# Performance work log

Measured on AMD Instinct MI355X. Metric: run time of the kernel, lower is better.

Reference implementation:

```python
import jax, jax.numpy as jnp
import numpy as np

V = 256        # vocab (bytes)
DM = 1024      # d_model
NL = 8         # num layers
N = 16         # d_state
K = 4          # d_conv
E = 2 * DM     # d_inner (expand=2)
R = DM // 16   # dt_rank = 64
EPS = 1e-5
B, T = 1, 1024


def setup_inputs() -> dict:
    key = jax.random.key(0)
    ks = jax.random.split(key, 10)
    s = lambda i, shape, scale=0.02: jax.random.normal(ks[i], shape, jnp.float32) * scale
    A_init = jnp.log(jnp.tile(jnp.arange(1, N + 1, dtype=jnp.float32), (NL, E, 1)))
    return {
        "input_ids": jax.random.randint(ks[0], (B, T), 0, V),
        "embed": s(1, (V, DM)),
        "Wxz": s(2, (NL, DM, 2 * E)),            # in_proj (no bias)
        "conv_w": s(3, (NL, E, K), 0.1),          # depthwise causal conv
        "conv_b": jnp.zeros((NL, E), jnp.float32),
        "Wx": s(4, (NL, E, R + 2 * N)),           # x_proj -> dt, B, C
        "Wdt": s(5, (NL, R, E), 0.1),             # dt_proj
        "dt_bias": jnp.full((NL, E), -4.6, jnp.float32),  # softplus(-4.6) ~ 0.01
        "A_log": A_init,                          # A = -exp(A_log), S4D-real init
        "D": jnp.ones((NL, E), jnp.float32),      # skip connection
        "Wout": s(6, (NL, E, DM)),                # out_proj (no bias)
        "norm_w": jnp.ones((NL, DM), jnp.float32),
        "final_norm_w": jnp.ones((DM,), jnp.float32),
        "lm_head_w": s(7, (DM, V)),               # lm_head (no bias)
    }


def rmsnorm(x, w):
    return x * jax.lax.rsqrt(jnp.mean(x * x, axis=-1, keepdims=True) + EPS) * w


def selective_scan(x, dt, A, Bm, Cm, Dp):
    # x, dt: [B,T,E]; A: [E,N]; Bm, Cm: [B,T,N]; Dp: [E]
    dA = jnp.exp(dt[..., None] * A)                              # [B,T,E,N]
    dBx = dt[..., None] * Bm[:, :, None, :] * x[..., None]       # [B,T,E,N]

    def step(h, inp):
        dA_t, dBx_t, C_t = inp                                   # [B,E,N],[B,E,N],[B,N]
        h = dA_t * h + dBx_t
        y = jnp.einsum('ben,bn->be', h, C_t)
        return h, y

    h0 = jnp.zeros((x.shape[0], E, N), x.dtype)
    _, ys = jax.lax.scan(step, h0, (dA.transpose(1, 0, 2, 3),
                                    dBx.transpose(1, 0, 2, 3),
                                    Cm.transpose(1, 0, 2)))
    return ys.transpose(1, 0, 2) + Dp * x                        # [B,T,E]


def mamba_layer(h, p):
    Wxz, cw, cb, Wx, Wdt, dtb, A_log, Dp, Wout, nw = p
    res = h
    u = rmsnorm(h, nw)
    xz = u @ Wxz                                                 # [B,T,2E]
    x, z = jnp.split(xz, 2, axis=-1)
    # causal depthwise conv over time
    xc = jax.lax.conv_general_dilated(x.transpose(0, 2, 1), cw[:, None, :],
                                      (1,), [(K - 1, 0)], feature_group_count=E)
    x = jax.nn.silu(xc.transpose(0, 2, 1) + cb)                  # [B,T,E]
    xdbl = x @ Wx                                                # [B,T,R+2N]
    dt = jax.nn.softplus(xdbl[..., :R] @ Wdt + dtb)              # [B,T,E]
    Bm = xdbl[..., R:R + N]
    Cm = xdbl[..., R + N:]
    A = -jnp.exp(A_log)                                          # [E,N]
    y = selective_scan(x, dt, A, Bm, Cm, Dp)
    y = y * jax.nn.silu(z)
    return res + y @ Wout, None


def reference(input_ids, embed, Wxz, conv_w, conv_b, Wx, Wdt, dt_bias, A_log, D,
              Wout, norm_w, final_norm_w, lm_head_w):
    h = embed[input_ids]                                         # [B,T,DM]
    h, _ = jax.lax.scan(mamba_layer, h,
                        (Wxz, conv_w, conv_b, Wx, Wdt, dt_bias, A_log, D, Wout, norm_w))
    h = rmsnorm(h, final_norm_w)
    return h @ lm_head_w                                         # logits [B,T,V]
```

## Files before the change

### kernel.cpp

```cpp
#include <hip/hip_runtime.h>
#include <hip/hip_bf16.h>

#define DM_   1024
#define NLAY  8
#define NST   16
#define KCONV 4
#define EE    2048
#define E2    4096
#define RNK   64
#define SEQ   1024
#define NXD   96
#define VOC   256
#define EPS_  1e-5f
#define NCH   32
#define CLEN  32

typedef __attribute__((ext_vector_type(8))) short bf16x8;
typedef __attribute__((ext_vector_type(4))) float f32x4;
typedef __hip_bfloat16 bf16;

__device__ __forceinline__ float sigmoidf_(float x){ return 1.f/(1.f+__expf(-x)); }
__device__ __forceinline__ float siluf_(float x){ return x*sigmoidf_(x); }
__device__ __forceinline__ float softplusf_(float x){ return (x>15.f)?x:log1pf(__expf(x)); }

__device__ __forceinline__ void gld_lds16(const short* g, short* lds_uniform){
  __builtin_amdgcn_global_load_lds(
      (const __attribute__((address_space(1))) unsigned int*)(const void*)g,
      (__attribute__((address_space(3))) unsigned int*)(void*)lds_uniform,
      16, 0, 0);
}

__global__ void k_transpose_bf16(const float* __restrict__ in, bf16* __restrict__ out,
                                 int rows, int cols, long in_stride, long out_stride){
  __shared__ float tile[32][33];
  const float* inp = in + (size_t)blockIdx.z * in_stride;
  bf16* outp = out + (size_t)blockIdx.z * out_stride;
  int c0 = blockIdx.x*32, r0 = blockIdx.y*32;
  int tx = threadIdx.x, ty = threadIdx.y;
#pragma unroll
  for (int j = 0; j < 4; j++)
    tile[ty + j*8][tx] = inp[(size_t)(r0 + ty + j*8)*cols + c0 + tx];
  __syncthreads();
#pragma unroll
  for (int j = 0; j < 4; j++)
    outp[(size_t)(c0 + ty + j*8)*rows + r0 + tx] = __float2bfloat16(tile[tx][ty + j*8]);
}

__global__ void k_rmsnorm_fuse(const int* __restrict__ ids, const float* __restrict__ emb,
                               float* __restrict__ h, const float* __restrict__ s0,
                               const float* __restrict__ s1, const float* __restrict__ w,
                               bf16* __restrict__ u){
  int t = blockIdx.x;
  float* hp = h + (size_t)t*DM_;
  float v[4];
  float ss = 0.f;
#pragma unroll
  for (int j = 0; j < 4; j++){
    int i = threadIdx.x + j*256;
    float x;
    if (ids){ x = emb[(size_t)ids[t]*DM_ + i]; hp[i] = x; }
    else if (s0){ x = hp[i] + s0[(size_t)t*DM_ + i] + s1[(size_t)t*DM_ + i]; hp[i] = x; }
    else { x = hp[i]; }
    v[j] = x; ss += x*x;
  }
#pragma unroll
  for (int o = 32; o > 0; o >>= 1) ss += __shfl_down(ss, o, 64);
  __shared__ float red[4];
  if ((threadIdx.x & 63) == 0) red[threadIdx.x >> 6] = ss;
  __syncthreads();
  float tot = red[0]+red[1]+red[2]+red[3];
  float sc = rsqrtf(tot*(1.f/DM_) + EPS_);
  bf16* up = u + (size_t)t*DM_;
#pragma unroll
  for (int j = 0; j < 4; j++){
    int i = threadIdx.x + j*256;
    up[i] = __float2bfloat16(v[j]*sc*w[i]);
  }
}

template<int BM, int BN, int NWM, int NWN, int MODE>
__global__ __launch_bounds__(256) void k_gemm(
    const short* __restrict__ A, const short* __restrict__ Bt, float* __restrict__ C,
    int M, int N, int K, int Ksplit, const float* __restrict__ bias)
{
  constexpr int BK = 64;
  constexpr int WM = BM/NWM, WN = BN/NWN;
  constexpr int MT = WM/16, NT = WN/16;
  constexpr int ABY = BM*BK*2, BBY = BN*BK*2;
  constexpr int AISS = ABY/4096, BISS = BBY/4096;
  __shared__ __align__(16) short As[2][BM*BK];
  __shared__ __align__(16) short Bs[2][BN*BK];
  int tid = threadIdx.x, lane = tid & 63, wave = tid >> 6;
  int wr = wave / NWN, wc = wave % NWN;
  int m0 = blockIdx.x * BM, n0 = blockIdx.y * BN;
  int lrow = lane & 15, lq = lane >> 4;
  int wbase = (tid & ~63) * 16;

  int kbeg = blockIdx.z * Ksplit;
  int nk = Ksplit / BK;

  f32x4 acc[MT][NT];
#pragma unroll
  for (int i = 0; i < MT; i++)
#pragma unroll
    for (int j = 0; j < NT; j++) acc[i][j] = (f32x4){0.f,0.f,0.f,0.f};

  auto stage = [&](int k0, int buf){
#pragma unroll
    for (int i = 0; i < AISS; i++){
      int off = i*4096 + tid*16;
      int row = off >> 7;
      int kc  = ((off >> 4) & 7) ^ (row & 7);
      gld_lds16(A + (size_t)(m0+row)*K + k0 + kc*8,
                As[buf] + ((i*4096 + wbase) >> 1));
    }
#pragma unroll
    for (int i = 0; i < BISS; i++){
      int off = i*4096 + tid*16;
      int row = off >> 7;
      int kc  = ((off >> 4) & 7) ^ (row & 7);
      gld_lds16(Bt + (size_t)(n0+row)*K + k0 + kc*8,
                Bs[buf] + ((i*4096 + wbase) >> 1));
    }
  };

  stage(kbeg, 0);
  __syncthreads();
  for (int it = 0; it < nk; it++){
    int cur = it & 1;
    if (it + 1 < nk) stage(kbeg + (it+1)*BK, cur ^ 1);
#pragma unroll
    for (int s = 0; s < 2; s++){
      bf16x8 af[MT], bfr[NT];
#pragma unroll
      for (int mt = 0; mt < MT; mt++){
        int row = wr*WM + mt*16 + lrow;
        int cc = (s*4 + lq) ^ (row & 7);
        af[mt] = *(const bf16x8*)(As[cur] + row*BK + cc*8);
      }
#pragma unroll
      for (int nt = 0; nt < NT; nt++){
        int row = wc*WN + nt*16 + lrow;
        int cc = (s*4 + lq) ^ (row & 7);
        bfr[nt] = *(const bf16x8*)(Bs[cur] + row*BK + cc*8);
      }
#pragma unroll
      for (int mt = 0; mt < MT; mt++)
#pragma unroll
        for (int nt = 0; nt < NT; nt++)
          acc[mt][nt] = __builtin_amdgcn_mfma_f32_16x16x32_bf16(af[mt], bfr[nt], acc[mt][nt], 0,0,0);
    }
    __syncthreads();
  }

  size_t slab = (MODE == 4) ? (size_t)blockIdx.z * M * N : 0;
#pragma unroll
  for (int mt = 0; mt < MT; mt++){
    int row = m0 + wr*WM + mt*16 + lq*4;
#pragma unroll
    for (int nt = 0; nt < NT; nt++){
      int col = n0 + wc*WN + nt*16 + lrow;
#pragma unroll
      for (int r = 0; r < 4; r++){
        float v = acc[mt][nt][r];
        size_t idx = slab + (size_t)(row + r)*N + col;
        if (MODE == 1) C[idx] = softplusf_(v + bias[col]);
        else C[idx] = v;
      }
    }
  }
}

__global__ void k_conv_silu(const float* __restrict__ xz, const float* __restrict__ cw,
                            const float* __restrict__ cb, float* __restrict__ xact,
                            bf16* __restrict__ xbf){
  int t = blockIdx.y;
  int e = blockIdx.x*256 + threadIdx.x;
  float4 w4 = *(const float4*)(cw + (size_t)e*4);
  float acc = cb[e];
  if (t >= 3){
    acc += xz[(size_t)(t-3)*E2 + e]*w4.x + xz[(size_t)(t-2)*E2 + e]*w4.y
         + xz[(size_t)(t-1)*E2 + e]*w4.z + xz[(size_t)t*E2 + e]*w4.w;
  } else {
    const float* wp = (const float*)&w4;
#pragma unroll
    for (int k = 0; k < 4; k++){ int tt = t-3+k; if (tt >= 0) acc += xz[(size_t)tt*E2 + e]*wp[k]; }
  }
  float xv = siluf_(acc);
  xact[(size_t)t*EE + e] = xv;
  xbf[(size_t)t*EE + e] = __float2bfloat16(xv);
}

__global__ void k_reduce_xdbl(const float* __restrict__ s, float* __restrict__ out,
                              bf16* __restrict__ out64){
  int i = blockIdx.x*256 + threadIdx.x;
  float v = 0.f;
#pragma unroll
  for (int c = 0; c < 8; c++) v += s[(size_t)c*SEQ*NXD + i];
  out[i] = v;
  int t = i / NXD, cc = i - t*NXD;
  if (cc < RNK) out64[(size_t)t*RNK + cc] = __float2bfloat16(v);
}

__global__ void k_reduce_lm(const float* __restrict__ s, float* __restrict__ out){
  int i = blockIdx.x*256 + threadIdx.x;
  float v = 0.f;
#pragma unroll
  for (int c = 0; c < 4; c++) v += s[(size_t)c*SEQ*VOC + i];
  out[i] = v;
}

__global__ void k_scanA(const float* __restrict__ dt, const float* __restrict__ x,
                        const float* __restrict__ xdbl, const float* __restrict__ Alog,
                        float* __restrict__ S, float* __restrict__ dtsum){
  int e = blockIdx.x*256 + threadIdx.x;
  int c = blockIdx.y;
  int t0 = c*CLEN;
  float Ae[NST];
#pragma unroll
  for (int n = 0; n < NST; n++) Ae[n] = -__expf(Alog[(size_t)e*NST + n]);
  __shared__ float Bsm[CLEN][NST];
  for (int i = threadIdx.x; i < CLEN*NST; i += 256)
    Bsm[i>>4][i&15] = xdbl[(size_t)(t0 + (i>>4))*NXD + RNK + (i&15)];
  __syncthreads();
  float h[NST];
#pragma unroll
  for (int n = 0; n < NST; n++) h[n] = 0.f;
  float ds = 0.f;
  for (int tt = 0; tt < CLEN; tt++){
    float dtv = dt[(size_t)(t0+tt)*EE + e];
    float xv  = x[(size_t)(t0+tt)*EE + e];
    ds += dtv;
    float sx = dtv * xv;
#pragma unroll
    for (int n = 0; n < NST; n++)
      h[n] = __expf(dtv*Ae[n])*h[n] + sx*Bsm[tt][n];
  }
  float* Sp = S + ((size_t)c*EE + e)*NST;
#pragma unroll
  for (int n = 0; n < NST; n++) Sp[n] = h[n];
  dtsum[(size_t)c*EE + e] = ds;
}

__global__ void k_scanB(const float* __restrict__ S, const float* __restrict__ dtsum,
                        const float* __restrict__ Alog, float* __restrict__ hinit){
  int idx = blockIdx.x*256 + threadIdx.x;
  float An = -__expf(Alog[idx]);
  int e = idx >> 4;
  float h = 0.f;
  for (int c = 0; c < NCH; c++){
    hinit[(size_t)c*EE*NST + idx] = h;
    h = __expf(dtsum[(size_t)c*EE + e]*An)*h + S[(size_t)c*EE*NST + idx];
  }
}

__global__ void k_scanC(const float* __restrict__ dt, const float* __restrict__ x,
                        const float* __restrict__ xdbl, const float* __restrict__ Alog,
                        const float* __restrict__ Dp, const float* __restrict__ hinit,
                        const float* __restrict__ xz, bf16* __restrict__ ybf){
  int e = blockIdx.x*256 + threadIdx.x;
  int c = blockIdx.y;
  int t0 = c*CLEN;
  float Ae[NST];
#pragma unroll
  for (int n = 0; n < NST; n++) Ae[n] = -__expf(Alog[(size_t)e*NST + n]);
  __shared__ float Bsm[CLEN][NST], Csm[CLEN][NST];
  for (int i = threadIdx.x; i < CLEN*NST; i += 256){
    int tt = i>>4, n = i&15;
    Bsm[tt][n] = xdbl[(size_t)(t0+tt)*NXD + RNK + n];
    Csm[tt][n] = xdbl[(size_t)(t0+tt)*NXD + RNK + NST + n];
  }
  __syncthreads();
  float h[NST];
  const float* hp = hinit + ((size_t)c*EE + e)*NST;
#pragma unroll
  for (int n = 0; n < NST; n++) h[n] = hp[n];
  float Dv = Dp[e];
  for (int tt = 0; tt < CLEN; tt++){
    float dtv = dt[(size_t)(t0+tt)*EE + e];
    float xv  = x[(size_t)(t0+tt)*EE + e];
    float sx = dtv*xv;
    float y = Dv*xv;
#pragma unroll
    for (int n = 0; n < NST; n++){
      h[n] = __expf(dtv*Ae[n])*h[n] + sx*Bsm[tt][n];
      y += h[n]*Csm[tt][n];
    }
    float zv = xz[(size_t)(t0+tt)*E2 + EE + e];
    y *= zv*sigmoidf_(zv);
    ybf[(size_t)(t0+tt)*EE + e] = __float2bfloat16(y);
  }
}

extern "C" void kernel_launch(void* const* d_in, const int* in_sizes, int n_in,
                              void* d_out, int out_size, void* d_ws, size_t ws_size,
                              hipStream_t stream)
{
  const int*   ids  = (const int*)d_in[0];
  const float* emb  = (const float*)d_in[1];
  const float* Wxz  = (const float*)d_in[2];
  const float* cw   = (const float*)d_in[3];
  const float* cb   = (const float*)d_in[4];
  const float* Wx   = (const float*)d_in[5];
  const float* Wdt  = (const float*)d_in[6];
  const float* dtb  = (const float*)d_in[7];
  const float* Alog = (const float*)d_in[8];
  const float* Dp   = (const float*)d_in[9];
  const float* Wout = (const float*)d_in[10];
  const float* nw   = (const float*)d_in[11];
  const float* fnw  = (const float*)d_in[12];
  const float* lmw  = (const float*)d_in[13];

  char* p = (char*)d_ws;
  auto alloc = [&](size_t bytes){ void* r = (void*)p; p += (bytes + 255) & ~(size_t)255; return r; };
  bf16* wxz_bf  = (bf16*)alloc((size_t)NLAY*E2*DM_*2);
  bf16* wout_bf = (bf16*)alloc((size_t)NLAY*DM_*EE*2);
  bf16* wx_bf   = (bf16*)alloc((size_t)NLAY*NXD*EE*2);
  bf16* wdt_bf  = (bf16*)alloc((size_t)NLAY*EE*RNK*2);
  bf16* lm_bf   = (bf16*)alloc((size_t)VOC*DM_*2);
  float* h      = (float*)alloc((size_t)SEQ*DM_*4);
  float* hslab  = (float*)alloc((size_t)2*SEQ*DM_*4);
  bf16* u_bf    = (bf16*)alloc((size_t)SEQ*DM_*2);
  float* xzb    = (float*)alloc((size_t)SEQ*E2*4);
  float* xact   = (float*)alloc((size_t)SEQ*EE*4);
  bf16* x_bf    = (bf16*)alloc((size_t)SEQ*EE*2);
  float* xdbl_s = (float*)alloc((size_t)8*SEQ*NXD*4);
  float* xdbl   = (float*)alloc((size_t)SEQ*NXD*4);
  bf16* xd64    = (bf16*)alloc((size_t)SEQ*RNK*2);
  float* dtbuf  = (float*)alloc((size_t)SEQ*EE*4);
  float* Sbuf   = (float*)alloc((size_t)NCH*EE*NST*4);
  float* dtsum  = (float*)alloc((size_t)NCH*EE*4);
  float* hinit  = (float*)alloc((size_t)NCH*EE*NST*4);
  bf16* y_bf    = (bf16*)alloc((size_t)SEQ*EE*2);
  float* lmslab = (float*)alloc((size_t)4*SEQ*VOC*4);

  k_transpose_bf16<<<dim3(E2/32, DM_/32, NLAY), dim3(32,8), 0, stream>>>(Wxz, wxz_bf, DM_, E2, (long)DM_*E2, (long)E2*DM_);
  k_transpose_bf16<<<dim3(DM_/32, EE/32, NLAY), dim3(32,8), 0, stream>>>(Wout, wout_bf, EE, DM_, (long)EE*DM_, (long)DM_*EE);
  k_transpose_bf16<<<dim3(NXD/32, EE/32, NLAY), dim3(32,8), 0, stream>>>(Wx, wx_bf, EE, NXD, (long)EE*NXD, (long)NXD*EE);
  k_transpose_bf16<<<dim3(EE/32, RNK/32, NLAY), dim3(32,8), 0, stream>>>(Wdt, wdt_bf, RNK, EE, (long)RNK*EE, (long)EE*RNK);
  k_transpose_bf16<<<dim3(VOC/32, DM_/32, 1), dim3(32,8), 0, stream>>>(lmw, lm_bf, DM_, VOC, 0, 0);

  for (int l = 0; l < NLAY; l++){
    k_rmsnorm_fuse<<<SEQ, 256, 0, stream>>>(
        l == 0 ? ids : nullptr, emb, h,
        l == 0 ? nullptr : hslab, hslab + (size_t)SEQ*DM_,
        nw + (size_t)l*DM_, u_bf);
    k_gemm<128,64,2,2,0><<<dim3(SEQ/128, E2/64, 1), 256, 0, stream>>>(
        (const short*)u_bf, (const short*)(wxz_bf + (size_t)l*E2*DM_), xzb,
        SEQ, E2, DM_, DM_, nullptr);
    k_conv_silu<<<dim3(EE/256, SEQ), 256, 0, stream>>>(
        xzb, cw + (size_t)l*EE*KCONV, cb + (size_t)l*EE, xact, x_bf);
    k_gemm<32,96,2,2,4><<<dim3(SEQ/32, 1, 8), 256, 0, stream>>>(
        (const short*)x_bf, (const short*)(wx_bf + (size_t)l*NXD*EE), xdbl_s,
        SEQ, NXD, EE, EE/8, nullptr);
    k_reduce_xdbl<<<SEQ*NXD/256, 256, 0, stream>>>(xdbl_s, xdbl, xd64);
    k_gemm<64,64,2,2,1><<<dim3(SEQ/64, EE/64, 1), 256, 0, stream>>>(
        (const short*)xd64, (const short*)(wdt_bf + (size_t)l*EE*RNK), dtbuf,
        SEQ, EE, RNK, RNK, dtb + (size_t)l*EE);
    k_scanA<<<dim3(EE/256, NCH), 256, 0, stream>>>(
        dtbuf, xact, xdbl, Alog + (size_t)l*EE*NST, Sbuf, dtsum);
    k_scanB<<<dim3(EE*NST/256), 256, 0, stream>>>(Sbuf, dtsum, Alog + (size_t)l*EE*NST, hinit);
    k_scanC<<<dim3(EE/256, NCH), 256, 0, stream>>>(
        dtbuf, xact, xdbl, Alog + (size_t)l*EE*NST, Dp + (size_t)l*EE, hinit, xzb, y_bf);
    k_gemm<64,64,2,2,4><<<dim3(SEQ/64, DM_/64, 2), 256, 0, stream>>>(
        (const short*)y_bf, (const short*)(wout_bf + (size_t)l*DM_*EE), hslab,
        SEQ, DM_, EE, EE/2, nullptr);
  }
  k_rmsnorm_fuse<<<SEQ, 256, 0, stream>>>(
      nullptr, emb, h, hslab, hslab + (size_t)SEQ*DM_, fnw, u_bf);
  k_gemm<64,64,2,2,4><<<dim3(SEQ/64, VOC/64, 4), 256, 0, stream>>>(
      (const short*)u_bf, (const short*)lm_bf, lmslab,
      SEQ, VOC, DM_, DM_/4, nullptr);
  k_reduce_lm<<<SEQ*VOC/256, 256, 0, stream>>>(lmslab, (float*)d_out);
}
```

Baseline: 1.164 ms.

## Replace per-stage kernel launches with a single cooperative persistent megakernel

```diff
diff --git a/kernel.cpp b/kernel.cpp
--- a/kernel.cpp
+++ b/kernel.cpp
@@ -1,10 +1,12 @@
 #include <hip/hip_runtime.h>
 #include <hip/hip_bf16.h>
+#include <hip/hip_cooperative_groups.h>
+
+namespace cg = cooperative_groups;
 
 #define DM_   1024
 #define NLAY  8
 #define NST   16
-#define KCONV 4
 #define EE    2048
 #define E2    4096
 #define RNK   64
@@ -12,16 +14,19 @@
 #define NXD   96
 #define VOC   256
 #define EPS_  1e-5f
-#define NCH   32
-#define CLEN  32
+#define NCH   64
+#define CLEN  16
+#define NTHR  256
 
 typedef __attribute__((ext_vector_type(8))) short bf16x8;
 typedef __attribute__((ext_vector_type(4))) float f32x4;
 typedef __hip_bfloat16 bf16;
 
 __device__ __forceinline__ float sigmoidf_(float x){ return 1.f/(1.f+__expf(-x)); }
-__device__ __forceinline__ float siluf_(float x){ return x*sigmoidf_(x); }
 __device__ __forceinline__ float softplusf_(float x){ return (x>15.f)?x:log1pf(__expf(x)); }
+__device__ __forceinline__ short f2bf_s(float x){
+  union { bf16 b; short s; } cv; cv.b = __float2bfloat16(x); return cv.s;
+}
 
 __device__ __forceinline__ void gld_lds16(const short* g, short* lds_uniform){
   __builtin_amdgcn_global_load_lds(
@@ -30,97 +35,110 @@
       16, 0, 0);
 }
 
-__global__ void k_transpose_bf16(const float* __restrict__ in, bf16* __restrict__ out,
-                                 int rows, int cols, long in_stride, long out_stride){
-  __shared__ float tile[32][33];
-  const float* inp = in + (size_t)blockIdx.z * in_stride;
-  bf16* outp = out + (size_t)blockIdx.z * out_stride;
-  int c0 = blockIdx.x*32, r0 = blockIdx.y*32;
-  int tx = threadIdx.x, ty = threadIdx.y;
-#pragma unroll
-  for (int j = 0; j < 4; j++)
-    tile[ty + j*8][tx] = inp[(size_t)(r0 + ty + j*8)*cols + c0 + tx];
-  __syncthreads();
-#pragma unroll
-  for (int j = 0; j < 4; j++)
-    outp[(size_t)(c0 + ty + j*8)*rows + r0 + tx] = __float2bfloat16(tile[tx][ty + j*8]);
-}
-
-__global__ void k_rmsnorm_fuse(const int* __restrict__ ids, const float* __restrict__ emb,
-                               float* __restrict__ h, const float* __restrict__ s0,
-                               const float* __restrict__ s1, const float* __restrict__ w,
-                               bf16* __restrict__ u){
-  int t = blockIdx.x;
-  float* hp = h + (size_t)t*DM_;
-  float v[4];
-  float ss = 0.f;
-#pragma unroll
-  for (int j = 0; j < 4; j++){
-    int i = threadIdx.x + j*256;
-    float x;
-    if (ids){ x = emb[(size_t)ids[t]*DM_ + i]; hp[i] = x; }
-    else if (s0){ x = hp[i] + s0[(size_t)t*DM_ + i] + s1[(size_t)t*DM_ + i]; hp[i] = x; }
-    else { x = hp[i]; }
-    v[j] = x; ss += x*x;
-  }
-#pragma unroll
-  for (int o = 32; o > 0; o >>= 1) ss += __shfl_down(ss, o, 64);
-  __shared__ float red[4];
-  if ((threadIdx.x & 63) == 0) red[threadIdx.x >> 6] = ss;
-  __syncthreads();
-  float tot = red[0]+red[1]+red[2]+red[3];
-  float sc = rsqrtf(tot*(1.f/DM_) + EPS_);
-  bf16* up = u + (size_t)t*DM_;
-#pragma unroll
-  for (int j = 0; j < 4; j++){
-    int i = threadIdx.x + j*256;
-    up[i] = __float2bfloat16(v[j]*sc*w[i]);
-  }
-}
-
-template<int BM, int BN, int NWM, int NWN, int MODE>
-__global__ __launch_bounds__(256) void k_gemm(
-    const short* __restrict__ A, const short* __restrict__ Bt, float* __restrict__ C,
-    int M, int N, int K, int Ksplit, const float* __restrict__ bias)
+struct Params {
+  const int* ids; const float* emb; const float* Wxz; const float* cw; const float* cb;
+  const float* Wx; const float* Wdt; const float* dtb; const float* Alog; const float* Dp;
+  const float* Wout; const float* nw; const float* fnw; const float* lmw;
+  bf16 *wxz_bf, *wout_bf, *wx_bf, *wdt_bf, *lm_bf;
+  float *h, *hslab; bf16 *u_bf;
+  float *xzb, *xact; bf16 *x_bf;
+  float *xdbl, *dtbuf, *S, *dtsum;
+  bf16 *y_bf; float *out;
+};
+
+__device__ void t_job(const float* in, bf16* out, int R, int C, int L, char* smem, int gdim){
+  float (*tile)[33] = (float(*)[33])smem;
+  int tC = C >> 5, tR = R >> 5;
+  int per = tC * tR, total = per * L;
+  int tx = threadIdx.x & 31, ty = threadIdx.x >> 5;
+  for (int it = blockIdx.x; it < total; it += gdim){
+    int l = it / per, rem = it - l*per;
+    int tc = rem % tC, tr = rem / tC;
+    const float* inp = in + (size_t)l*R*C;
+    bf16* outp = out + (size_t)l*R*C;
+    int c0 = tc*32, r0 = tr*32;
+    __syncthreads();
+#pragma unroll
+    for (int j = 0; j < 4; j++)
+      tile[ty + j*8][tx] = inp[(size_t)(r0+ty+j*8)*C + c0+tx];
+    __syncthreads();
+#pragma unroll
+    for (int j = 0; j < 4; j++)
+      outp[(size_t)(c0+ty+j*8)*R + r0+tx] = __float2bfloat16(tile[tx][ty+j*8]);
+  }
+}
+
+__device__ void rms_phase(const Params& P, int mode, char* smem, int gdim){
+  float* red = (float*)smem;
+  const float* w = (mode == NLAY) ? P.fnw : (P.nw + (size_t)mode*DM_);
+  int tid = threadIdx.x;
+  for (int t = blockIdx.x; t < SEQ; t += gdim){
+    float* hp = P.h + (size_t)t*DM_;
+    float v[4]; float ss = 0.f;
+    __syncthreads();
+#pragma unroll
+    for (int j = 0; j < 4; j++){
+      int i = tid + j*256;
+      float x;
+      if (mode == 0){ x = P.emb[(size_t)P.ids[t]*DM_ + i]; hp[i] = x; }
+      else { x = hp[i] + P.hslab[(size_t)t*DM_ + i] + P.hslab[(size_t)(SEQ+t)*DM_ + i]; hp[i] = x; }
+      v[j] = x; ss += x*x;
+    }
+#pragma unroll
+    for (int o = 32; o > 0; o >>= 1) ss += __shfl_down(ss, o, 64);
+    if ((tid & 63) == 0) red[tid >> 6] = ss;
+    __syncthreads();
+    float sc = rsqrtf((red[0]+red[1]+red[2]+red[3])*(1.f/DM_) + EPS_);
+    bf16* up = P.u_bf + (size_t)t*DM_;
+#pragma unroll
+    for (int j = 0; j < 4; j++){
+      int i = tid + j*256;
+      up[i] = __float2bfloat16(v[j]*sc*w[i]);
+    }
+  }
+  if (mode == NLAY){
+    int stride = gdim*NTHR;
+    for (int i = blockIdx.x*NTHR + tid; i < SEQ*VOC; i += stride) P.out[i] = 0.f;
+  }
+}
+
+template<int BM,int BN,int NWM,int NWN>
+__device__ __forceinline__ void gemm_core(
+    const short* __restrict__ A, const short* __restrict__ Bt, int K,
+    int m0, int n0, int kbeg, int nk, short* As, short* Bs,
+    f32x4 (&acc)[(BM/NWM)/16][(BN/NWN)/16])
 {
   constexpr int BK = 64;
   constexpr int WM = BM/NWM, WN = BN/NWN;
   constexpr int MT = WM/16, NT = WN/16;
   constexpr int ABY = BM*BK*2, BBY = BN*BK*2;
   constexpr int AISS = ABY/4096, BISS = BBY/4096;
-  __shared__ __align__(16) short As[2][BM*BK];
-  __shared__ __align__(16) short Bs[2][BN*BK];
-  int tid = threadIdx.x, lane = tid & 63, wave = tid >> 6;
-  int wr = wave / NWN, wc = wave % NWN;
-  int m0 = blockIdx.x * BM, n0 = blockIdx.y * BN;
-  int lrow = lane & 15, lq = lane >> 4;
-  int wbase = (tid & ~63) * 16;
-
-  int kbeg = blockIdx.z * Ksplit;
-  int nk = Ksplit / BK;
-
-  f32x4 acc[MT][NT];
+  const int tid = threadIdx.x, lane = tid & 63, wave = tid >> 6;
+  const int wr = wave / NWN, wc = wave % NWN;
+  const int lrow = lane & 15, lq = lane >> 4;
+  const int wbase = (tid & ~63) * 16;
+
 #pragma unroll
   for (int i = 0; i < MT; i++)
 #pragma unroll
     for (int j = 0; j < NT; j++) acc[i][j] = (f32x4){0.f,0.f,0.f,0.f};
 
   auto stage = [&](int k0, int buf){
+    short* Ad = As + buf*(BM*BK);
+    short* Bd = Bs + buf*(BN*BK);
 #pragma unroll
     for (int i = 0; i < AISS; i++){
       int off = i*4096 + tid*16;
       int row = off >> 7;
       int kc  = ((off >> 4) & 7) ^ (row & 7);
-      gld_lds16(A + (size_t)(m0+row)*K + k0 + kc*8,
-                As[buf] + ((i*4096 + wbase) >> 1));
+      gld_lds16(A + (size_t)(m0+row)*K + k0 + kc*8, Ad + ((i*4096 + wbase) >> 1));
     }
 #pragma unroll
     for (int i = 0; i < BISS; i++){
       int off = i*4096 + tid*16;
       int row = off >> 7;
       int kc  = ((off >> 4) & 7) ^ (row & 7);
-      gld_lds16(Bt + (size_t)(n0+row)*K + k0 + kc*8,
-                Bs[buf] + ((i*4096 + wbase) >> 1));
+      gld_lds16(Bt + (size_t)(n0+row)*K + k0 + kc*8, Bd + ((i*4096 + wbase) >> 1));
     }
   };
 
@@ -129,6 +147,8 @@
   for (int it = 0; it < nk; it++){
     int cur = it & 1;
     if (it + 1 < nk) stage(kbeg + (it+1)*BK, cur ^ 1);
+    const short* Ac = As + cur*(BM*BK);
+    const short* Bc = Bs + cur*(BN*BK);
 #pragma unroll
     for (int s = 0; s < 2; s++){
       bf16x8 af[MT], bfr[NT];
@@ -136,13 +156,13 @@
       for (int mt = 0; mt < MT; mt++){
         int row = wr*WM + mt*16 + lrow;
         int cc = (s*4 + lq) ^ (row & 7);
-        af[mt] = *(const bf16x8*)(As[cur] + row*BK + cc*8);
+        af[mt] = *(const bf16x8*)(Ac + row*BK + cc*8);
       }
 #pragma unroll
       for (int nt = 0; nt < NT; nt++){
         int row = wc*WN + nt*16 + lrow;
         int cc = (s*4 + lq) ^ (row & 7);
-        bfr[nt] = *(const bf16x8*)(Bs[cur] + row*BK + cc*8);
+        bfr[nt] = *(const bf16x8*)(Bc + row*BK + cc*8);
       }
 #pragma unroll
       for (int mt = 0; mt < MT; mt++)
@@ -152,224 +172,360 @@
     }
     __syncthreads();
   }
-
-  size_t slab = (MODE == 4) ? (size_t)blockIdx.z * M * N : 0;
-#pragma unroll
-  for (int mt = 0; mt < MT; mt++){
-    int row = m0 + wr*WM + mt*16 + lq*4;
-#pragma unroll
-    for (int nt = 0; nt < NT; nt++){
-      int col = n0 + wc*WN + nt*16 + lrow;
-#pragma unroll
-      for (int r = 0; r < 4; r++){
-        float v = acc[mt][nt][r];
-        size_t idx = slab + (size_t)(row + r)*N + col;
-        if (MODE == 1) C[idx] = softplusf_(v + bias[col]);
-        else C[idx] = v;
-      }
-    }
-  }
-}
-
-__global__ void k_conv_silu(const float* __restrict__ xz, const float* __restrict__ cw,
-                            const float* __restrict__ cb, float* __restrict__ xact,
-                            bf16* __restrict__ xbf){
-  int t = blockIdx.y;
-  int e = blockIdx.x*256 + threadIdx.x;
-  float4 w4 = *(const float4*)(cw + (size_t)e*4);
-  float acc = cb[e];
-  if (t >= 3){
-    acc += xz[(size_t)(t-3)*E2 + e]*w4.x + xz[(size_t)(t-2)*E2 + e]*w4.y
-         + xz[(size_t)(t-1)*E2 + e]*w4.z + xz[(size_t)t*E2 + e]*w4.w;
-  } else {
-    const float* wp = (const float*)&w4;
-#pragma unroll
-    for (int k = 0; k < 4; k++){ int tt = t-3+k; if (tt >= 0) acc += xz[(size_t)tt*E2 + e]*wp[k]; }
-  }
-  float xv = siluf_(acc);
-  xact[(size_t)t*EE + e] = xv;
-  xbf[(size_t)t*EE + e] = __float2bfloat16(xv);
-}
-
-__global__ void k_reduce_xdbl(const float* __restrict__ s, float* __restrict__ out,
-                              bf16* __restrict__ out64){
-  int i = blockIdx.x*256 + threadIdx.x;
-  float v = 0.f;
-#pragma unroll
-  for (int c = 0; c < 8; c++) v += s[(size_t)c*SEQ*NXD + i];
-  out[i] = v;
-  int t = i / NXD, cc = i - t*NXD;
-  if (cc < RNK) out64[(size_t)t*RNK + cc] = __float2bfloat16(v);
-}
-
-__global__ void k_reduce_lm(const float* __restrict__ s, float* __restrict__ out){
-  int i = blockIdx.x*256 + threadIdx.x;
-  float v = 0.f;
-#pragma unroll
-  for (int c = 0; c < 4; c++) v += s[(size_t)c*SEQ*VOC + i];
-  out[i] = v;
-}
-
-__global__ void k_scanA(const float* __restrict__ dt, const float* __restrict__ x,
-                        const float* __restrict__ xdbl, const float* __restrict__ Alog,
-                        float* __restrict__ S, float* __restrict__ dtsum){
-  int e = blockIdx.x*256 + threadIdx.x;
-  int c = blockIdx.y;
-  int t0 = c*CLEN;
-  float Ae[NST];
-#pragma unroll
-  for (int n = 0; n < NST; n++) Ae[n] = -__expf(Alog[(size_t)e*NST + n]);
-  __shared__ float Bsm[CLEN][NST];
-  for (int i = threadIdx.x; i < CLEN*NST; i += 256)
-    Bsm[i>>4][i&15] = xdbl[(size_t)(t0 + (i>>4))*NXD + RNK + (i&15)];
-  __syncthreads();
-  float h[NST];
-#pragma unroll
-  for (int n = 0; n < NST; n++) h[n] = 0.f;
-  float ds = 0.f;
-  for (int tt = 0; tt < CLEN; tt++){
-    float dtv = dt[(size_t)(t0+tt)*EE + e];
-    float xv  = x[(size_t)(t0+tt)*EE + e];
-    ds += dtv;
-    float sx = dtv * xv;
-#pragma unroll
-    for (int n = 0; n < NST; n++)
-      h[n] = __expf(dtv*Ae[n])*h[n] + sx*Bsm[tt][n];
-  }
-  float* Sp = S + ((size_t)c*EE + e)*NST;
-#pragma unroll
-  for (int n = 0; n < NST; n++) Sp[n] = h[n];
-  dtsum[(size_t)c*EE + e] = ds;
-}
-
-__global__ void k_scanB(const float* __restrict__ S, const float* __restrict__ dtsum,
-                        const float* __restrict__ Alog, float* __restrict__ hinit){
-  int idx = blockIdx.x*256 + threadIdx.x;
-  float An = -__expf(Alog[idx]);
-  int e = idx >> 4;
-  float h = 0.f;
-  for (int c = 0; c < NCH; c++){
-    hinit[(size_t)c*EE*NST + idx] = h;
-    h = __expf(dtsum[(size_t)c*EE + e]*An)*h + S[(size_t)c*EE*NST + idx];
-  }
-}
-
-__global__ void k_scanC(const float* __restrict__ dt, const float* __restrict__ x,
-                        const float* __restrict__ xdbl, const float* __restrict__ Alog,
-                        const float* __restrict__ Dp, const float* __restrict__ hinit,
-                        const float* __restrict__ xz, bf16* __restrict__ ybf){
-  int e = blockIdx.x*256 + threadIdx.x;
-  int c = blockIdx.y;
-  int t0 = c*CLEN;
-  float Ae[NST];
-#pragma unroll
-  for (int n = 0; n < NST; n++) Ae[n] = -__expf(Alog[(size_t)e*NST + n]);
-  __shared__ float Bsm[CLEN][NST], Csm[CLEN][NST];
-  for (int i = threadIdx.x; i < CLEN*NST; i += 256){
-    int tt = i>>4, n = i&15;
-    Bsm[tt][n] = xdbl[(size_t)(t0+tt)*NXD + RNK + n];
-    Csm[tt][n] = xdbl[(size_t)(t0+tt)*NXD + RNK + NST + n];
-  }
-  __syncthreads();
-  float h[NST];
-  const float* hp = hinit + ((size_t)c*EE + e)*NST;
-#pragma unroll
-  for (int n = 0; n < NST; n++) h[n] = hp[n];
-  float Dv = Dp[e];
-  for (int tt = 0; tt < CLEN; tt++){
-    float dtv = dt[(size_t)(t0+tt)*EE + e];
-    float xv  = x[(size_t)(t0+tt)*EE + e];
-    float sx = dtv*xv;
-    float y = Dv*xv;
-#pragma unroll
-    for (int n = 0; n < NST; n++){
-      h[n] = __expf(dtv*Ae[n])*h[n] + sx*Bsm[tt][n];
-      y += h[n]*Csm[tt][n];
-    }
-    float zv = xz[(size_t)(t0+tt)*E2 + EE + e];
-    y *= zv*sigmoidf_(zv);
-    ybf[(size_t)(t0+tt)*EE + e] = __float2bfloat16(y);
-  }
+}
+
+__device__ void wxz_phase(const Params& P, int l, char* smem, int gdim){
+  short* As = (short*)smem;
+  short* Bs = (short*)(smem + 16384);
+  const short* A  = (const short*)P.u_bf;
+  const short* Bt = (const short*)(P.wxz_bf + (size_t)l*E2*DM_);
+  int lane = threadIdx.x & 63, wave = threadIdx.x >> 6;
+  int wr = wave >> 1, wc = wave & 1, lrow = lane & 15, lq = lane >> 4;
+  for (int tile = blockIdx.x; tile < 16*64; tile += gdim){
+    int mi = tile >> 6, ni = tile & 63;
+    f32x4 acc[2][2];
+    gemm_core<64,64,2,2>(A, Bt, DM_, mi*64, ni*64, 0, DM_/64, As, Bs, acc);
+#pragma unroll
+    for (int mt = 0; mt < 2; mt++){
+      int row = mi*64 + wr*32 + mt*16 + lq*4;
+#pragma unroll
+      for (int nt = 0; nt < 2; nt++){
+        int col = ni*64 + wc*32 + nt*16 + lrow;
+#pragma unroll
+        for (int r = 0; r < 4; r++)
+          P.xzb[(size_t)(row+r)*E2 + col] = acc[mt][nt][r];
+      }
+    }
+  }
+}
+
+__device__ void conv_phase(const Params& P, int l, int gdim){
+  int stride = gdim*NTHR;
+  int gtid = blockIdx.x*NTHR + threadIdx.x;
+  const float* cwl = P.cw + (size_t)l*EE*4;
+  const float* cbl = P.cb + (size_t)l*EE;
+  for (int idx = gtid; idx < SEQ*EE; idx += stride){
+    int t = idx >> 11, e = idx & 2047;
+    float4 w4 = *(const float4*)(cwl + (size_t)e*4);
+    float acc = cbl[e];
+    const float* col = P.xzb + e;
+    if (t >= 3){
+      acc += col[(size_t)(t-3)*E2]*w4.x + col[(size_t)(t-2)*E2]*w4.y
+           + col[(size_t)(t-1)*E2]*w4.z + col[(size_t)t*E2]*w4.w;
+    } else {
+      const float* wp = (const float*)&w4;
+#pragma unroll
+      for (int k = 0; k < 4; k++){ int tt = t-3+k; if (tt >= 0) acc += col[(size_t)tt*E2]*wp[k]; }
+    }
+    float xv = acc * sigmoidf_(acc);
+    P.xact[idx] = xv;
+    P.x_bf[idx] = __float2bfloat16(xv);
+  }
+  for (int i = gtid; i < SEQ*NXD; i += stride) P.xdbl[i] = 0.f;
+}
+
+__device__ void wx_phase(const Params& P, int l, char* smem, int gdim){
+  short* As = (short*)smem;
+  short* Bs = (short*)(smem + 8192);
+  const short* A  = (const short*)P.x_bf;
+  const short* Bt = (const short*)(P.wx_bf + (size_t)l*NXD*EE);
+  int lane = threadIdx.x & 63, wave = threadIdx.x >> 6;
+  int wr = wave >> 1, wc = wave & 1, lrow = lane & 15, lq = lane >> 4;
+  for (int tile = blockIdx.x; tile < 512; tile += gdim){
+    int z = tile & 15, mi = tile >> 4;
+    f32x4 acc[1][3];
+    gemm_core<32,96,2,2>(A, Bt, EE, mi*32, 0, z*128, 2, As, Bs, acc);
+    int row = mi*32 + wr*16 + lq*4;
+#pragma unroll
+    for (int nt = 0; nt < 3; nt++){
+      int col = wc*48 + nt*16 + lrow;
+#pragma unroll
+      for (int r = 0; r < 4; r++)
+        atomicAdd(&P.xdbl[(size_t)(row+r)*NXD + col], acc[0][nt][r]);
+    }
+  }
+}
+
+__device__ void dt_phase(const Params& P, int l, char* smem, int gdim){
+  short* As = (short*)smem;
+  short* Bs = (short*)(smem + 8192);
+  int tid = threadIdx.x;
+  int lane = tid & 63, wave = tid >> 6;
+  int wr = wave >> 1, wc = wave & 1, lrow = lane & 15, lq = lane >> 4;
+  const short* Bt = (const short*)(P.wdt_bf + (size_t)l*EE*RNK);
+  const float* bias = P.dtb + (size_t)l*EE;
+  for (int tile = blockIdx.x; tile < 512; tile += gdim){
+    int mi = tile >> 5, ni = tile & 31;
+    int m0 = mi*64, n0 = ni*64;
+    __syncthreads();
+    {
+      int row = tid >> 2;
+      int kq  = (tid & 3) << 4;
+      const float* src = P.xdbl + (size_t)(m0+row)*NXD + kq;
+      short tmp[16] __attribute__((aligned(16)));
+#pragma unroll
+      for (int j = 0; j < 16; j++) tmp[j] = f2bf_s(src[j]);
+      int c0 = ((kq>>3) + 0) ^ (row & 7);
+      int c1 = ((kq>>3) + 1) ^ (row & 7);
+      *(bf16x8*)(As + row*64 + c0*8) = *(const bf16x8*)(tmp);
+      *(bf16x8*)(As + row*64 + c1*8) = *(const bf16x8*)(tmp + 8);
+    }
+    {
+      int wbase = (tid & ~63) * 16;
+#pragma unroll
+      for (int i = 0; i < 2; i++){
+        int off = i*4096 + tid*16;
+        int row = off >> 7;
+        int kc  = ((off >> 4) & 7) ^ (row & 7);
+        gld_lds16(Bt + (size_t)(n0+row)*RNK + kc*8, Bs + ((i*4096 + wbase) >> 1));
+      }
+    }
+    __syncthreads();
+    f32x4 acc[2][2];
+#pragma unroll
+    for (int i = 0; i < 2; i++)
+#pragma unroll
+      for (int j = 0; j < 2; j++) acc[i][j] = (f32x4){0.f,0.f,0.f,0.f};
+#pragma unroll
+    for (int s = 0; s < 2; s++){
+      bf16x8 af[2], bfr[2];
+#pragma unroll
+      for (int mt = 0; mt < 2; mt++){
+        int row = wr*32 + mt*16 + lrow;
+        int cc = (s*4 + lq) ^ (row & 7);
+        af[mt] = *(const bf16x8*)(As + row*64 + cc*8);
+      }
+#pragma unroll
+      for (int nt = 0; nt < 2; nt++){
+        int row = wc*32 + nt*16 + lrow;
+        int cc = (s*4 + lq) ^ (row & 7);
+        bfr[nt] = *(const bf16x8*)(Bs + row*64 + cc*8);
+      }
+#pragma unroll
+      for (int mt = 0; mt < 2; mt++)
+#pragma unroll
+        for (int nt = 0; nt < 2; nt++)
+          acc[mt][nt] = __builtin_amdgcn_mfma_f32_16x16x32_bf16(af[mt], bfr[nt], acc[mt][nt], 0,0,0);
+    }
+#pragma unroll
+    for (int mt = 0; mt < 2; mt++){
+      int row = m0 + wr*32 + mt*16 + lq*4;
+#pragma unroll
+      for (int nt = 0; nt < 2; nt++){
+        int col = n0 + wc*32 + nt*16 + lrow;
+#pragma unroll
+        for (int r = 0; r < 4; r++)
+          P.dtbuf[(size_t)(row+r)*EE + col] = softplusf_(acc[mt][nt][r] + bias[col]);
+      }
+    }
+  }
+}
+
+__device__ void scanA_phase(const Params& P, int l, char* smem, int gdim){
+  float (*Bsm)[NST] = (float(*)[NST])smem;
+  for (int b = blockIdx.x; b < 512; b += gdim){
+    int eg = b & 7, c = b >> 3;
+    int e = eg*256 + threadIdx.x;
+    int t0 = c*CLEN;
+    const float* Al = P.Alog + (size_t)l*EE*NST + (size_t)e*NST;
+    float Ae[NST];
+#pragma unroll
+    for (int n = 0; n < NST; n++) Ae[n] = -__expf(Al[n]);
+    __syncthreads();
+    { int i = threadIdx.x; Bsm[i>>4][i&15] = P.xdbl[(size_t)(t0+(i>>4))*NXD + RNK + (i&15)]; }
+    __syncthreads();
+    float h[NST];
+#pragma unroll
+    for (int n = 0; n < NST; n++) h[n] = 0.f;
+    float ds = 0.f;
+    for (int tt = 0; tt < CLEN; tt++){
+      float dtv = P.dtbuf[(size_t)(t0+tt)*EE + e];
+      float xv  = P.xact[(size_t)(t0+tt)*EE + e];
+      ds += dtv;
+      float sx = dtv*xv;
+#pragma unroll
+      for (int n = 0; n < NST; n++)
+        h[n] = __expf(dtv*Ae[n])*h[n] + sx*Bsm[tt][n];
+    }
+    float* Sp = P.S + ((size_t)c*EE + e)*NST;
+#pragma unroll
+    for (int n = 0; n < NST; n++) Sp[n] = h[n];
+    P.dtsum[(size_t)c*EE + e] = ds;
+  }
+}
+
+__device__ void scanC_phase(const Params& P, int l, char* smem, int gdim){
+  float (*Bsm)[NST] = (float(*)[NST])smem;
+  float (*Csm)[NST] = (float(*)[NST])(smem + CLEN*NST*4);
+  for (int b = blockIdx.x; b < 512; b += gdim){
+    int eg = b & 7, c = b >> 3;
+    int e = eg*256 + threadIdx.x;
+    int t0 = c*CLEN;
+    const float* Al = P.Alog + (size_t)l*EE*NST + (size_t)e*NST;
+    float Ae[NST];
+#pragma unroll
+    for (int n = 0; n < NST; n++) Ae[n] = -__expf(Al[n]);
+    __syncthreads();
+    { int i = threadIdx.x; int tt = i>>4, n = i&15;
+      Bsm[tt][n] = P.xdbl[(size_t)(t0+tt)*NXD + RNK + n];
+      Csm[tt][n] = P.xdbl[(size_t)(t0+tt)*NXD + RNK + NST + n]; }
+    __syncthreads();
+    float h[NST];
+#pragma unroll
+    for (int n = 0; n < NST; n++) h[n] = 0.f;
+#pragma unroll 1
+    for (int j = 0; j < c; j++){
+      float dsj = P.dtsum[(size_t)j*EE + e];
+      const float* Sj = P.S + ((size_t)j*EE + e)*NST;
+#pragma unroll
+      for (int n = 0; n < NST; n++)
+        h[n] = __expf(dsj*Ae[n])*h[n] + Sj[n];
+    }
+    float Dv = P.Dp[(size_t)l*EE + e];
+    for (int tt = 0; tt < CLEN; tt++){
+      float dtv = P.dtbuf[(size_t)(t0+tt)*EE + e];
+      float xv  = P.xact[(size_t)(t0+tt)*EE + e];
+      float sx = dtv*xv;
+      float y = Dv*xv;
+#pragma unroll
+      for (int n = 0; n < NST; n++){
+        h[n] = __expf(dtv*Ae[n])*h[n] + sx*Bsm[tt][n];
+        y += h[n]*Csm[tt][n];
+      }
+      float zv = P.xzb[(size_t)(t0+tt)*E2 + EE + e];
+      y *= zv*sigmoidf_(zv);
+      P.y_bf[(size_t)(t0+tt)*EE + e] = __float2bfloat16(y);
+    }
+  }
+}
+
+__device__ void wout_phase(const Params& P, int l, char* smem, int gdim){
+  short* As = (short*)smem;
+  short* Bs = (short*)(smem + 16384);
+  const short* A  = (const short*)P.y_bf;
+  const short* Bt = (const short*)(P.wout_bf + (size_t)l*DM_*EE);
+  int lane = threadIdx.x & 63, wave = threadIdx.x >> 6;
+  int wr = wave >> 1, wc = wave & 1, lrow = lane & 15, lq = lane >> 4;
+  for (int tile = blockIdx.x; tile < 512; tile += gdim){
+    int z = tile & 1, mi = (tile >> 1) & 15, ni = (tile >> 5) & 15;
+    f32x4 acc[2][2];
+    gemm_core<64,64,2,2>(A, Bt, EE, mi*64, ni*64, z*1024, 16, As, Bs, acc);
+    float* dst = P.hslab + (size_t)z*SEQ*DM_;
+#pragma unroll
+    for (int mt = 0; mt < 2; mt++){
+      int row = mi*64 + wr*32 + mt*16 + lq*4;
+#pragma unroll
+      for (int nt = 0; nt < 2; nt++){
+        int col = ni*64 + wc*32 + nt*16 + lrow;
+#pragma unroll
+        for (int r = 0; r < 4; r++)
+          dst[(size_t)(row+r)*DM_ + col] = acc[mt][nt][r];
+      }
+    }
+  }
+}
+
+__device__ void lm_phase(const Params& P, char* smem, int gdim){
+  short* As = (short*)smem;
+  short* Bs = (short*)(smem + 16384);
+  const short* A  = (const short*)P.u_bf;
+  const short* Bt = (const short*)P.lm_bf;
+  int lane = threadIdx.x & 63, wave = threadIdx.x >> 6;
+  int wr = wave >> 1, wc = wave & 1, lrow = lane & 15, lq = lane >> 4;
+  for (int tile = blockIdx.x; tile < 512; tile += gdim){
+    int z = tile & 7, mi = (tile >> 3) & 15, ni = tile >> 7;
+    f32x4 acc[2][2];
+    gemm_core<64,64,2,2>(A, Bt, DM_, mi*64, ni*64, z*128, 2, As, Bs, acc);
+#pragma unroll
+    for (int mt = 0; mt < 2; mt++){
+      int row = mi*64 + wr*32 + mt*16 + lq*4;
+#pragma unroll
+      for (int nt = 0; nt < 2; nt++){
+        int col = ni*64 + wc*32 + nt*16 + lrow;
+#pragma unroll
+        for (int r = 0; r < 4; r++)
+          atomicAdd(&P.out[(size_t)(row+r)*VOC + col], acc[mt][nt][r]);
+      }
+    }
+  }
+}
+
+__global__ __launch_bounds__(256,2) void k_mega(Params P){
+  cg::grid_group grid = cg::this_grid();
+  __shared__ __align__(16) char smem[32768];
+  int gdim = gridDim.x;
+
+  t_job(P.Wxz,  P.wxz_bf,  DM_, E2,  NLAY, smem, gdim);
+  t_job(P.Wout, P.wout_bf, EE,  DM_, NLAY, smem, gdim);
+  t_job(P.Wx,   P.wx_bf,   EE,  NXD, NLAY, smem, gdim);
+  t_job(P.Wdt,  P.wdt_bf,  RNK, EE,  NLAY, smem, gdim);
+  t_job(P.lmw,  P.lm_bf,   DM_, VOC, 1,    smem, gdim);
+  rms_phase(P, 0, smem, gdim);
+  grid.sync();
+
+  for (int l = 0; l < NLAY; l++){
+    if (l > 0){ rms_phase(P, l, smem, gdim); grid.sync(); }
+    wxz_phase(P, l, smem, gdim);   grid.sync();
+    conv_phase(P, l, gdim);        grid.sync();
+    wx_phase(P, l, smem, gdim);    grid.sync();
+    dt_phase(P, l, smem, gdim);    grid.sync();
+    scanA_phase(P, l, smem, gdim); grid.sync();
+    scanC_phase(P, l, smem, gdim); grid.sync();
+    wout_phase(P, l, smem, gdim);  grid.sync();
+  }
+  rms_phase(P, NLAY, smem, gdim);
+  grid.sync();
+  lm_phase(P, smem, gdim);
 }
 
 extern "C" void kernel_launch(void* const* d_in, const int* in_sizes, int n_in,
                               void* d_out, int out_size, void* d_ws, size_t ws_size,
                               hipStream_t stream)
 {
-  const int*   ids  = (const int*)d_in[0];
-  const float* emb  = (const float*)d_in[1];
-  const float* Wxz  = (const float*)d_in[2];
-  const float* cw   = (const float*)d_in[3];
-  const float* cb   = (const float*)d_in[4];
-  const float* Wx   = (const float*)d_in[5];
-  const float* Wdt  = (const float*)d_in[6];
-  const float* dtb  = (const float*)d_in[7];
-  const float* Alog = (const float*)d_in[8];
-  const float* Dp   = (const float*)d_in[9];
-  const float* Wout = (const float*)d_in[10];
-  const float* nw   = (const float*)d_in[11];
-  const float* fnw  = (const float*)d_in[12];
-  const float* lmw  = (const float*)d_in[13];
+  Params pa;
+  pa.ids  = (const int*)d_in[0];
+  pa.emb  = (const float*)d_in[1];
+  pa.Wxz  = (const float*)d_in[2];
+  pa.cw   = (const float*)d_in[3];
+  pa.cb   = (const float*)d_in[4];
+  pa.Wx   = (const float*)d_in[5];
+  pa.Wdt  = (const float*)d_in[6];
+  pa.dtb  = (const float*)d_in[7];
+  pa.Alog = (const float*)d_in[8];
+  pa.Dp   = (const float*)d_in[9];
+  pa.Wout = (const float*)d_in[10];
+  pa.nw   = (const float*)d_in[11];
+  pa.fnw  = (const float*)d_in[12];
+  pa.lmw  = (const float*)d_in[13];
 
   char* p = (char*)d_ws;
   auto alloc = [&](size_t bytes){ void* r = (void*)p; p += (bytes + 255) & ~(size_t)255; return r; };
-  bf16* wxz_bf  = (bf16*)alloc((size_t)NLAY*E2*DM_*2);
-  bf16* wout_bf = (bf16*)alloc((size_t)NLAY*DM_*EE*2);
-  bf16* wx_bf   = (bf16*)alloc((size_t)NLAY*NXD*EE*2);
-  bf16* wdt_bf  = (bf16*)alloc((size_t)NLAY*EE*RNK*2);
-  bf16* lm_bf   = (bf16*)alloc((size_t)VOC*DM_*2);
-  float* h      = (float*)alloc((size_t)SEQ*DM_*4);
-  float* hslab  = (float*)alloc((size_t)2*SEQ*DM_*4);
-  bf16* u_bf    = (bf16*)alloc((size_t)SEQ*DM_*2);
-  float* xzb    = (float*)alloc((size_t)SEQ*E2*4);
-  float* xact   = (float*)alloc((size_t)SEQ*EE*4);
-  bf16* x_bf    = (bf16*)alloc((size_t)SEQ*EE*2);
-  float* xdbl_s = (float*)alloc((size_t)8*SEQ*NXD*4);
-  float* xdbl   = (float*)alloc((size_t)SEQ*NXD*4);
-  bf16* xd64    = (bf16*)alloc((size_t)SEQ*RNK*2);
-  float* dtbuf  = (float*)alloc((size_t)SEQ*EE*4);
-  float* Sbuf   = (float*)alloc((size_t)NCH*EE*NST*4);
-  float* dtsum  = (float*)alloc((size_t)NCH*EE*4);
-  float* hinit  = (float*)alloc((size_t)NCH*EE*NST*4);
-  bf16* y_bf    = (bf16*)alloc((size_t)SEQ*EE*2);
-  float* lmslab = (float*)alloc((size_t)4*SEQ*VOC*4);
-
-  k_transpose_bf16<<<dim3(E2/32, DM_/32, NLAY), dim3(32,8), 0, stream>>>(Wxz, wxz_bf, DM_, E2, (long)DM_*E2, (long)E2*DM_);
-  k_transpose_bf16<<<dim3(DM_/32, EE/32, NLAY), dim3(32,8), 0, stream>>>(Wout, wout_bf, EE, DM_, (long)EE*DM_, (long)DM_*EE);
-  k_transpose_bf16<<<dim3(NXD/32, EE/32, NLAY), dim3(32,8), 0, stream>>>(Wx, wx_bf, EE, NXD, (long)EE*NXD, (long)NXD*EE);
-  k_transpose_bf16<<<dim3(EE/32, RNK/32, NLAY), dim3(32,8), 0, stream>>>(Wdt, wdt_bf, RNK, EE, (long)RNK*EE, (long)EE*RNK);
-  k_transpose_bf16<<<dim3(VOC/32, DM_/32, 1), dim3(32,8), 0, stream>>>(lmw, lm_bf, DM_, VOC, 0, 0);
-
-  for (int l = 0; l < NLAY; l++){
-    k_rmsnorm_fuse<<<SEQ, 256, 0, stream>>>(
-        l == 0 ? ids : nullptr, emb, h,
-        l == 0 ? nullptr : hslab, hslab + (size_t)SEQ*DM_,
-        nw + (size_t)l*DM_, u_bf);
-    k_gemm<128,64,2,2,0><<<dim3(SEQ/128, E2/64, 1), 256, 0, stream>>>(
-        (const short*)u_bf, (const short*)(wxz_bf + (size_t)l*E2*DM_), xzb,
-        SEQ, E2, DM_, DM_, nullptr);
-    k_conv_silu<<<dim3(EE/256, SEQ), 256, 0, stream>>>(
-        xzb, cw + (size_t)l*EE*KCONV, cb + (size_t)l*EE, xact, x_bf);
-    k_gemm<32,96,2,2,4><<<dim3(SEQ/32, 1, 8), 256, 0, stream>>>(
-        (const short*)x_bf, (const short*)(wx_bf + (size_t)l*NXD*EE), xdbl_s,
-        SEQ, NXD, EE, EE/8, nullptr);
-    k_reduce_xdbl<<<SEQ*NXD/256, 256, 0, stream>>>(xdbl_s, xdbl, xd64);
-    k_gemm<64,64,2,2,1><<<dim3(SEQ/64, EE/64, 1), 256, 0, stream>>>(
-        (const short*)xd64, (const short*)(wdt_bf + (size_t)l*EE*RNK), dtbuf,
-        SEQ, EE, RNK, RNK, dtb + (size_t)l*EE);
-    k_scanA<<<dim3(EE/256, NCH), 256, 0, stream>>>(
-        dtbuf, xact, xdbl, Alog + (size_t)l*EE*NST, Sbuf, dtsum);
-    k_scanB<<<dim3(EE*NST/256), 256, 0, stream>>>(Sbuf, dtsum, Alog + (size_t)l*EE*NST, hinit);
-    k_scanC<<<dim3(EE/256, NCH), 256, 0, stream>>>(
-        dtbuf, xact, xdbl, Alog + (size_t)l*EE*NST, Dp + (size_t)l*EE, hinit, xzb, y_bf);
-    k_gemm<64,64,2,2,4><<<dim3(SEQ/64, DM_/64, 2), 256, 0, stream>>>(
-        (const short*)y_bf, (const short*)(wout_bf + (size_t)l*DM_*EE), hslab,
-        SEQ, DM_, EE, EE/2, nullptr);
-  }
-  k_rmsnorm_fuse<<<SEQ, 256, 0, stream>>>(
-      nullptr, emb, h, hslab, hslab + (size_t)SEQ*DM_, fnw, u_bf);
-  k_gemm<64,64,2,2,4><<<dim3(SEQ/64, VOC/64, 4), 256, 0, stream>>>(
-      (const short*)u_bf, (const short*)lm_bf, lmslab,
-      SEQ, VOC, DM_, DM_/4, nullptr);
-  k_reduce_lm<<<SEQ*VOC/256, 256, 0, stream>>>(lmslab, (float*)d_out);
-}
+  pa.wxz_bf  = (bf16*)alloc((size_t)NLAY*E2*DM_*2);
+  pa.wout_bf = (bf16*)alloc((size_t)NLAY*DM_*EE*2);
+  pa.wx_bf   = (bf16*)alloc((size_t)NLAY*NXD*EE*2);
+  pa.wdt_bf  = (bf16*)alloc((size_t)NLAY*EE*RNK*2);
+  pa.lm_bf   = (bf16*)alloc((size_t)VOC*DM_*2);
+  pa.h       = (float*)alloc((size_t)SEQ*DM_*4);
+  pa.hslab   = (float*)alloc((size_t)2*SEQ*DM_*4);
+  pa.u_bf    = (bf16*)alloc((size_t)SEQ*DM_*2);
+  pa.xzb     = (float*)alloc((size_t)SEQ*E2*4);
+  pa.xact    = (float*)alloc((size_t)SEQ*EE*4);
+  pa.x_bf    = (bf16*)alloc((size_t)SEQ*EE*2);
+  pa.xdbl    = (float*)alloc((size_t)SEQ*NXD*4);
+  pa.dtbuf   = (float*)alloc((size_t)SEQ*EE*4);
+  pa.S       = (float*)alloc((size_t)NCH*EE*NST*4);
+  pa.dtsum   = (float*)alloc((size_t)NCH*EE*4);
+  pa.y_bf    = (bf16*)alloc((size_t)SEQ*EE*2);
+  pa.out     = (float*)d_out;
+
+  int dev = 0; hipGetDevice(&dev);
+  int cus = 0; hipDeviceGetAttribute(&cus, hipDeviceAttributeMultiprocessorCount, dev);
+  int occ = 0; hipOccupancyMaxActiveBlocksPerMultiprocessor(&occ, (const void*)k_mega, NTHR, 0);
+  if (occ < 1) occ = 1;
+  if (cus < 1) cus = 256;
+  long grid = (long)cus * occ;
+  if (grid > 512) grid = 512;
+
+  void* args[] = { &pa };
+  hipLaunchCooperativeKernel((const void*)k_mega, dim3((int)grid), dim3(NTHR), args, 0, stream);
+}
```

Measured after the change: 3.681 ms. +216.1%, slower.
